# Optimization experiments

Measured on AMD Instinct MI355X. Metric: run time of the kernel, lower is better.

Reference implementation:

```python
import jax, jax.numpy as jnp
import numpy as np

B, T = 4, 2048
OBS, ST = 512, 512
H, E = 8, 64

def setup_inputs() -> dict:
    key = jax.random.key(0)
    k1, k2, k3, k4, k5 = jax.random.split(key, 5)
    observe = jax.random.normal(k1, (B, T, OBS), dtype=jnp.float32)
    state = jax.random.normal(k2, (B, T, ST), dtype=jnp.float32)
    # nn.Linear weights (out, in) applied as x @ W.T; store transposed for einsum
    Wq = jax.random.normal(k3, (OBS, H * E), dtype=jnp.float32) * (1.0 / np.sqrt(OBS))
    Wk = jax.random.normal(k4, (ST, H * E), dtype=jnp.float32) * (1.0 / np.sqrt(ST))
    Wv = jax.random.normal(k5, (ST, H * E), dtype=jnp.float32) * (1.0 / np.sqrt(ST))
    merge_w = jnp.ones((1, H, E), dtype=jnp.float32)  # Merger weight, init fill_(1.0)
    return {"observe": observe, "state": state, "Wq": Wq, "Wk": Wk, "Wv": Wv, "merge_w": merge_w}

def reference(observe, state, Wq, Wk, Wv, merge_w):
    b, t, _ = observe.shape
    h, e = H, E
    scale = e ** 0.25
    q = (observe @ Wq).reshape(b, t, h, e).transpose(0, 2, 1, 3) / scale  # [b,h,t,e]
    k = (state @ Wk).reshape(b, t, h, e).transpose(0, 2, 1, 3) / scale
    v = (state @ Wv).reshape(b, t, h, e).transpose(0, 2, 1, 3)
    dot = jnp.einsum('bhqe,bhke->bhqk', q, k)  # [b,h,t,t]
    attn = jax.nn.softmax(dot, axis=-1)
    out = jnp.einsum('bhqk,bhke->bhqe', attn, v)  # [b,h,t,e]
    out = out.transpose(0, 2, 1, 3).reshape(b * t, h, e)  # [b*t,h,e]
    # Merger: softmax over head dim of learned weight, weighted head sum
    w = jax.nn.softmax(merge_w, axis=1)  # [1,h,e]
    return jnp.sum(w * out, axis=1)  # [b*t,e]
```

## Files before the change

kernel.cpp:

```cpp
#include <hip/hip_runtime.h>

#define B_ 4
#define T_ 2048
#define H_ 8
#define E_ 64
#define KDIM 512

typedef unsigned short ushort_t;
typedef __attribute__((ext_vector_type(4))) float f32x4;
typedef __attribute__((ext_vector_type(4))) int i32x4;
typedef __attribute__((ext_vector_type(8))) short s16x8;

#define QK_SCALE 0.42466043f

__device__ __forceinline__ ushort_t f2bf(float f) {
  unsigned u = __builtin_bit_cast(unsigned, f);
  u += 0x7fffu + ((u >> 16) & 1u);
  return (ushort_t)(u >> 16);
}
__device__ __forceinline__ unsigned pk2(float a, float b) {
  return (unsigned)f2bf(a) | ((unsigned)f2bf(b) << 16);
}
__device__ __forceinline__ unsigned pk2t(float a, float b) {
  return __builtin_amdgcn_perm(__builtin_bit_cast(unsigned, b),
                               __builtin_bit_cast(unsigned, a), 0x07060302u);
}
__device__ __forceinline__ float e2(float x) { return __builtin_amdgcn_exp2f(x); }
__device__ __forceinline__ void gl2lds16(const void* g, void* l) {
  __builtin_amdgcn_global_load_lds((const __attribute__((address_space(1))) unsigned*)g,
                                   (__attribute__((address_space(3))) unsigned*)l, 16, 0, 0);
}

__global__ void k_prep(const float* __restrict__ Wq, const float* __restrict__ Wk,
                       const float* __restrict__ Wv, ushort_t* __restrict__ wt) {
  __shared__ ushort_t tile[64][66];
  int z = blockIdx.z;
  const float* W = (z == 0) ? Wq : (z == 1 ? Wk : Wv);
  float scale = (z < 2) ? QK_SCALE : 1.0f;
  int k0 = blockIdx.y << 6, n0 = blockIdx.x << 6;
  int rr = threadIdx.x >> 6, cc = threadIdx.x & 63;
  for (int p = 0; p < 16; p++) {
    int kl = p * 4 + rr;
    tile[cc][kl] = f2bf(W[(size_t)(k0 + kl) * 512 + n0 + cc] * scale);
  }
  __syncthreads();
  int kp2 = threadIdx.x & 31, nr = threadIdx.x >> 5;
  unsigned* wt32 = (unsigned*)(wt + (size_t)z * 262144);
  for (int p = 0; p < 8; p++) {
    int nl = p * 8 + nr;
    unsigned val = (unsigned)tile[nl][kp2 * 2] | ((unsigned)tile[nl][kp2 * 2 + 1] << 16);
    wt32[(size_t)(n0 + nl) * 256 + (k0 >> 1) + kp2] = val;
  }
}

__global__ void k_wgt(const float* __restrict__ mw, float* __restrict__ wgt) {
  int e = threadIdx.x;
  float w[8], wmax = -1e30f;
  for (int h = 0; h < 8; h++) { w[h] = mw[h * 64 + e]; wmax = fmaxf(wmax, w[h]); }
  float wsum = 0.f;
  for (int h = 0; h < 8; h++) { w[h] = __expf(w[h] - wmax); wsum += w[h]; }
  float inv = 1.f / wsum;
  for (int h = 0; h < 8; h++) wgt[h * 64 + e] = w[h] * inv;
}

__global__ void k_cvt(const float* __restrict__ obs, const float* __restrict__ st,
                      unsigned* __restrict__ xo, unsigned* __restrict__ xs) {
  int which = blockIdx.y;
  const float* src = which ? st : obs;
  unsigned* dst = which ? xs : xo;
  size_t idx = (size_t)blockIdx.x * 256 + threadIdx.x;
  size_t base = idx * 8;
  float4 x0 = *(const float4*)(src + base);
  float4 x1 = *(const float4*)(src + base + 4);
  uint4 d;
  d.x = pk2(x0.x, x0.y);
  d.y = pk2(x0.z, x0.w);
  d.z = pk2(x1.x, x1.y);
  d.w = pk2(x1.z, x1.w);
  *(uint4*)(dst + idx * 4) = d;
}

__global__ __launch_bounds__(256, 3) void k_proj2(
    const ushort_t* __restrict__ xo, const ushort_t* __restrict__ xs,
    const ushort_t* __restrict__ wt,
    ushort_t* __restrict__ qo, ushort_t* __restrict__ ko, ushort_t* __restrict__ vto) {
  __shared__ __align__(16) ushort_t As[2][128 * 64];

  int id = blockIdx.x;
  int xcd = id & 7, nt = (id >> 3) & 3, ghi = id >> 5;
  int g = ghi * 8 + xcd;
  int which = g >> 6, mb = g & 63;
  int m0 = mb << 7, n0 = nt << 7;
  const ushort_t* X = (which == 0) ? xo : xs;
  const ushort_t* W = wt + which * 262144;

  int tid = threadIdx.x, wave = tid >> 6, lane = tid & 63;
  int l15 = lane & 15, quad = lane >> 4;
  int wm = wave & 1, wn = wave >> 1;

  f32x4 acc[4][4];
  for (int i = 0; i < 4; i++)
    for (int j = 0; j < 4; j++) acc[i][j] = (f32x4){0.f, 0.f, 0.f, 0.f};

  int arl = lane >> 3, ap = lane & 7;

#define STAGEA(buf, k0)                                                            \
  do {                                                                             \
    for (int ii = 0; ii < 4; ii++) {                                               \
      int r = wave * 32 + ii * 8 + arl;                                            \
      gl2lds16(X + (size_t)(m0 + r) * KDIM + (k0) + ((ap ^ (r & 7)) << 3),         \
               &As[buf][(wave * 32 + ii * 8) * 64]);                               \
    }                                                                              \
  } while (0)

  const ushort_t* wb[4];
  for (int j = 0; j < 4; j++)
    wb[j] = W + (size_t)(n0 + wn * 64 + j * 16 + l15) * KDIM + quad * 8;

  STAGEA(0, 0);
  __builtin_amdgcn_s_waitcnt(0x0F70);
  __syncthreads();

  for (int kt = 0; kt < 8; kt++) {
    s16x8 b[2][4];
    for (int kc = 0; kc < 2; kc++)
      for (int j = 0; j < 4; j++) b[kc][j] = *(const s16x8*)(wb[j] + kc * 32);
    for (int j = 0; j < 4; j++) wb[j] += 64;
    if (kt < 7) STAGEA((kt + 1) & 1, kt * 64 + 64);
    const ushort_t* asb = As[kt & 1];
    for (int kc = 0; kc < 2; kc++) {
      s16x8 a[4];
      for (int i = 0; i < 4; i++) {
        int mr = wm * 64 + i * 16 + l15;
        int pc = (kc * 4 + quad) ^ (l15 & 7);
        a[i] = *(const s16x8*)&asb[mr * 64 + pc * 8];
      }
      if (which == 2) {
        for (int i = 0; i < 4; i++)
          for (int j = 0; j < 4; j++)
            acc[i][j] = __builtin_amdgcn_mfma_f32_16x16x32_bf16(b[kc][j], a[i], acc[i][j], 0, 0, 0);
      } else {
        for (int i = 0; i < 4; i++)
          for (int j = 0; j < 4; j++)
            acc[i][j] = __builtin_amdgcn_mfma_f32_16x16x32_bf16(a[i], b[kc][j], acc[i][j], 0, 0, 0);
      }
    }
    __builtin_amdgcn_s_waitcnt(0x0F70);
    __syncthreads();
  }
#undef STAGEA

  if (which != 2) {
    ushort_t* dst = (which == 0) ? qo : ko;
    for (int i = 0; i < 4; i++) {
      int grow = m0 + wm * 64 + i * 16 + quad * 4;
      for (int j = 0; j < 4; j++) {
        int gcol = n0 + wn * 64 + j * 16 + l15;
        int h = gcol >> 6, e = gcol & 63;
        for (int r = 0; r < 4; r++) {
          int row = grow + r;
          int bb = row >> 11, t = row & 2047;
          int bh = bb * H_ + h;
          dst[(((size_t)bh * T_ + t) << 6) + e] = f2bf(acc[i][j][r]);
        }
      }
    }
  } else {
    for (int i = 0; i < 4; i++) {
      int row = m0 + wm * 64 + i * 16 + l15;
      int bb = row >> 11, t = row & 2047;
      for (int j = 0; j < 4; j++) {
        for (int r = 0; r < 4; r++) {
          int gcol = n0 + wn * 64 + j * 16 + quad * 4 + r;
          int h = gcol >> 6, e = gcol & 63;
          int bh = bb * H_ + h;
          vto[((size_t)(bh << 6) + e) * T_ + t] = f2bf(acc[i][j][r]);
        }
      }
    }
  }
}

__global__ __launch_bounds__(256, 3) void k_proj(
    const float* __restrict__ obs, const float* __restrict__ st,
    const ushort_t* __restrict__ wt,
    ushort_t* __restrict__ qo, ushort_t* __restrict__ ko, ushort_t* __restrict__ vto) {
  __shared__ __align__(16) float As[2][128 * 32];

  int id = blockIdx.x;
  int xcd = id & 7, nt = (id >> 3) & 3, ghi = id >> 5;
  int g = ghi * 8 + xcd;
  int which = g >> 6, mb = g & 63;
  int m0 = mb << 7, n0 = nt << 7;
  const float* X = (which == 0) ? obs : st;
  const ushort_t* W = wt + which * 262144;

  int tid = threadIdx.x, wave = tid >> 6, lane = tid & 63;
  int l15 = lane & 15, quad = lane >> 4;
  int wm = wave & 1, wn = wave >> 1;

  f32x4 acc[4][4];
  for (int i = 0; i < 4; i++)
    for (int j = 0; j < 4; j++) acc[i][j] = (f32x4){0.f, 0.f, 0.f, 0.f};

  int arl = lane >> 3, ap = lane & 7;

#define STAGEA(buf, k0)                                                           \
  do {                                                                            \
    for (int ii = 0; ii < 4; ii++) {                                              \
      int r = wave * 32 + ii * 8 + arl;                                           \
      gl2lds16(X + (size_t)(m0 + r) * KDIM + (k0) + ((ap ^ (r & 7)) << 2),        \
               &As[buf][(wave * 32 + ii * 8) * 32]);                              \
    }                                                                             \
  } while (0)

  const ushort_t* wb[4];
  for (int j = 0; j < 4; j++)
    wb[j] = W + (size_t)(n0 + wn * 64 + j * 16 + l15) * KDIM + quad * 8;

  STAGEA(0, 0);
  __builtin_amdgcn_s_waitcnt(0x0F70);
  __syncthreads();

  for (int kt = 0; kt < 16; kt++) {
    s16x8 b[4];
    for (int j = 0; j < 4; j++) { b[j] = *(const s16x8*)wb[j]; wb[j] += 32; }
    if (kt < 15) STAGEA((kt + 1) & 1, kt * 32 + 32);
    const float* asb = As[kt & 1];
    s16x8 a[4];
    for (int i = 0; i < 4; i++) {
      int mr = wm * 64 + i * 16 + l15;
      int s = mr & 7;
      const float* rowp = &asb[mr * 32];
      float4 x0 = *(const float4*)&rowp[(((quad << 1)) ^ s) << 2];
      float4 x1 = *(const float4*)&rowp[(((quad << 1) | 1) ^ s) << 2];
      i32x4 d;
      d[0] = (int)pk2(x0.x, x0.y);
      d[1] = (int)pk2(x0.z, x0.w);
      d[2] = (int)pk2(x1.x, x1.y);
      d[3] = (int)pk2(x1.z, x1.w);
      a[i] = __builtin_bit_cast(s16x8, d);
    }
    if (which == 2) {
      for (int i = 0; i < 4; i++)
        for (int j = 0; j < 4; j++)
          acc[i][j] = __builtin_amdgcn_mfma_f32_16x16x32_bf16(b[j], a[i], acc[i][j], 0, 0, 0);
    } else {
      for (int i = 0; i < 4; i++)
        for (int j = 0; j < 4; j++)
          acc[i][j] = __builtin_amdgcn_mfma_f32_16x16x32_bf16(a[i], b[j], acc[i][j], 0, 0, 0);
    }
    __builtin_amdgcn_s_waitcnt(0x0F70);
    __syncthreads();
  }
#undef STAGEA

  if (which != 2) {
    ushort_t* dst = (which == 0) ? qo : ko;
    for (int i = 0; i < 4; i++) {
      int grow = m0 + wm * 64 + i * 16 + quad * 4;
      for (int j = 0; j < 4; j++) {
        int gcol = n0 + wn * 64 + j * 16 + l15;
        int h = gcol >> 6, e = gcol & 63;
        for (int r = 0; r < 4; r++) {
          int row = grow + r;
          int bb = row >> 11, t = row & 2047;
          int bh = bb * H_ + h;
          dst[(((size_t)bh * T_ + t) << 6) + e] = f2bf(acc[i][j][r]);
        }
      }
    }
  } else {
    for (int i = 0; i < 4; i++) {
      int row = m0 + wm * 64 + i * 16 + l15;
      int bb = row >> 11, t = row & 2047;
      for (int j = 0; j < 4; j++) {
        for (int r = 0; r < 4; r++) {
          int gcol = n0 + wn * 64 + j * 16 + quad * 4 + r;
          int h = gcol >> 6, e = gcol & 63;
          int bh = bb * H_ + h;
          vto[((size_t)(bh << 6) + e) * T_ + t] = f2bf(acc[i][j][r]);
        }
      }
    }
  }
}

union AttnSmem {
  struct { ushort_t ks[2][64 * 64]; ushort_t vs[2][64 * 64]; } st;
  struct { float ows[64 * 65]; float linv[64]; } ep;
};

__global__ __launch_bounds__(256, 4) void k_attn(
    const ushort_t* __restrict__ q, const ushort_t* __restrict__ k,
    const ushort_t* __restrict__ vt, const float* __restrict__ wgt,
    float* __restrict__ out) {
  __shared__ __align__(16) AttnSmem sm;

  int id = blockIdx.x;
  int bh = id & 31, qt = id >> 5;
  int tid = threadIdx.x, wave = tid >> 6, lane = tid & 63;
  int l15 = lane & 15, quad = lane >> 4;

  s16x8 qf[2][2];
  for (int qs = 0; qs < 2; qs++) {
    const ushort_t* qp =
        q + (((size_t)bh * T_ + qt * 128 + wave * 32 + qs * 16 + l15) << 6) + quad * 8;
    qf[qs][0] = *(const s16x8*)qp;
    qf[qs][1] = *(const s16x8*)(qp + 32);
  }
  int hh = bh & 7;
  float wgl = wgt[hh * 64 + lane];

  f32x4 o[2][4];
  for (int qs = 0; qs < 2; qs++)
    for (int j = 0; j < 4; j++) o[qs][j] = (f32x4){0.f, 0.f, 0.f, 0.f};
  f32x4 lacc[2] = {(f32x4){0.f, 0.f, 0.f, 0.f}, (f32x4){0.f, 0.f, 0.f, 0.f}};
  const s16x8 ones = {16256, 16256, 16256, 16256, 16256, 16256, 16256, 16256};

  int srl = lane >> 3, sp = lane & 7;
  const ushort_t* kbase = k + ((size_t)bh * T_ << 6);
  const ushort_t* vbase = vt + ((size_t)bh << 6) * T_;
  const ushort_t* kptr[2];
  const ushort_t* vptr[2];
  for (int ii = 0; ii < 2; ii++) {
    int r = wave * 16 + ii * 8 + srl;
    int gkey = (r & 32) + (((r >> 2) & 3) << 3) + (((r >> 4) & 1) << 2) + (r & 3);
    kptr[ii] = kbase + ((size_t)gkey << 6) + ((sp ^ (r & 7)) << 3);
    int e = r;
    vptr[ii] = vbase + (size_t)e * T_ + ((sp ^ (e & 7)) << 3);
  }

#define STAGE(buf)                                                         \
  do {                                                                     \
    for (int ii = 0; ii < 2; ii++) {                                       \
      gl2lds16(kptr[ii], &sm.st.ks[buf][(wave * 16 + ii * 8) * 64]);       \
      gl2lds16(vptr[ii], &sm.st.vs[buf][(wave * 16 + ii * 8) * 64]);       \
      kptr[ii] += 64 * 64;                                                 \
      vptr[ii] += 64;                                                      \
    }                                                                      \
  } while (0)

  STAGE(0);
  for (int kt = 0; kt < 32; kt++) {
    __builtin_amdgcn_s_waitcnt(0x0F70);
    __syncthreads();
    if (kt < 31) STAGE((kt + 1) & 1);
    const ushort_t* ksb = sm.st.ks[kt & 1];
    const ushort_t* vsb = sm.st.vs[kt & 1];

    s16x8 bfr[2][2];
    for (int c = 0; c < 2; c++) {
      f32x4 s0[2], s1[2];
      for (int qs = 0; qs < 2; qs++) {
        s0[qs] = (f32x4){0.f, 0.f, 0.f, 0.f};
        s1[qs] = (f32x4){0.f, 0.f, 0.f, 0.f};
      }
      for (int kc = 0; kc < 2; kc++) {
        int pc = (kc * 4 + quad) ^ (l15 & 7);
        s16x8 k0f = *(const s16x8*)&ksb[(c * 32 + l15) * 64 + pc * 8];
        s16x8 k1f = *(const s16x8*)&ksb[(c * 32 + 16 + l15) * 64 + pc * 8];
        for (int qs = 0; qs < 2; qs++) {
          s0[qs] = __builtin_amdgcn_mfma_f32_16x16x32_bf16(k0f, qf[qs][kc], s0[qs], 0, 0, 0);
          s1[qs] = __builtin_amdgcn_mfma_f32_16x16x32_bf16(k1f, qf[qs][kc], s1[qs], 0, 0, 0);
        }
      }
      for (int qs = 0; qs < 2; qs++) {
        i32x4 d;
        d[0] = (int)pk2t(e2(s0[qs][0]), e2(s0[qs][1]));
        d[1] = (int)pk2t(e2(s0[qs][2]), e2(s0[qs][3]));
        d[2] = (int)pk2t(e2(s1[qs][0]), e2(s1[qs][1]));
        d[3] = (int)pk2t(e2(s1[qs][2]), e2(s1[qs][3]));
        bfr[qs][c] = __builtin_bit_cast(s16x8, d);
      }
    }

    for (int c = 0; c < 2; c++) {
      lacc[0] = __builtin_amdgcn_mfma_f32_16x16x32_bf16(ones, bfr[0][c], lacc[0], 0, 0, 0);
      lacc[1] = __builtin_amdgcn_mfma_f32_16x16x32_bf16(ones, bfr[1][c], lacc[1], 0, 0, 0);
      for (int et = 0; et < 4; et++) {
        int pc = (c * 4 + quad) ^ (l15 & 7);
        s16x8 vf = *(const s16x8*)&vsb[(et * 16 + l15) * 64 + pc * 8];
        o[0][et] = __builtin_amdgcn_mfma_f32_16x16x32_bf16(vf, bfr[0][c], o[0][et], 0, 0, 0);
        o[1][et] = __builtin_amdgcn_mfma_f32_16x16x32_bf16(vf, bfr[1][c], o[1][et], 0, 0, 0);
      }
    }
  }
#undef STAGE

  int bb = bh >> 3;
  for (int half = 0; half < 2; half++) {
    __syncthreads();
    if ((wave >> 1) == half) {
      int tl = (wave & 1) * 32;
      for (int qs = 0; qs < 2; qs++) {
        int row = tl + qs * 16 + l15;
        if (quad == 0) sm.ep.linv[row] = 1.f / lacc[qs][0];
        for (int et = 0; et < 4; et++)
          for (int r = 0; r < 4; r++)
            sm.ep.ows[row * 65 + et * 16 + quad * 4 + r] = o[qs][et][r];
      }
    }
    __syncthreads();
    for (int i = 0; i < 16; i++) {
      int row = wave * 16 + i;
      int gt = qt * 128 + half * 64 + row;
      float val = sm.ep.ows[row * 65 + lane] * sm.ep.linv[row] * wgl;
      atomicAdd(&out[(((size_t)bb * T_ + gt) << 6) + lane], val);
    }
  }
}

extern "C" void kernel_launch(void* const* d_in, const int* in_sizes, int n_in,
                              void* d_out, int out_size, void* d_ws, size_t ws_size,
                              hipStream_t stream) {
  const float* obs = (const float*)d_in[0];
  const float* st  = (const float*)d_in[1];
  const float* Wq  = (const float*)d_in[2];
  const float* Wk  = (const float*)d_in[3];
  const float* Wv  = (const float*)d_in[4];
  const float* mw  = (const float*)d_in[5];

  const size_t WS_NEEDED = 27262976;
  const size_t WS_BIG    = 44040192;
  char* ws = (char*)d_ws;
  ushort_t* wt  = (ushort_t*)ws;
  float*    wgt = (float*)(ws + 1572864u);
  ushort_t* qo  = (ushort_t*)(ws + 2097152u);
  ushort_t* ko  = (ushort_t*)(ws + 10485760u);
  ushort_t* vto = (ushort_t*)(ws + 18874368u);
  ushort_t* xo  = (ushort_t*)(ws + 27262976u);
  ushort_t* xs  = (ushort_t*)(ws + 35651584u);
  float*    out = (float*)d_out;

  hipMemsetAsync(d_out, 0, (size_t)out_size * sizeof(float), stream);
  if (ws_size < WS_NEEDED) return;

  hipLaunchKernelGGL(k_prep, dim3(8, 8, 3), dim3(256), 0, stream, Wq, Wk, Wv, wt);
  hipLaunchKernelGGL(k_wgt,  dim3(1),       dim3(64),  0, stream, mw, wgt);
  if (ws_size >= WS_BIG) {
    hipLaunchKernelGGL(k_cvt,   dim3(2048, 2), dim3(256), 0, stream, obs, st,
                       (unsigned*)xo, (unsigned*)xs);
    hipLaunchKernelGGL(k_proj2, dim3(768),     dim3(256), 0, stream, xo, xs, wt, qo, ko, vto);
  } else {
    hipLaunchKernelGGL(k_proj,  dim3(768),     dim3(256), 0, stream, obs, st, wt, qo, ko, vto);
  }
  hipLaunchKernelGGL(k_attn, dim3(512), dim3(256), 0, stream, qo, ko, vto, wgt, out);
}
```

Before: 192.5 us.

## Triple-buffer LDS staging in projection and attention kernels with partial vmcnt waits

Both the projection GEMM and the attention kernel move from double to triple buffering of their LDS tiles, issuing loads two iterations ahead. They wait with a partial vmcnt so that only the oldest stage must land before the barrier, with raw s_barrier plus sched_barrier in place of __syncthreads. The goal is to hide more global-to-LDS latency behind MFMA work. In exchange LDS use grows, and the attention kernel's launch bounds drop from 4 to 2 blocks per CU, which may reduce occupancy.

```diff
diff --git a/kernel.cpp b/kernel.cpp
--- a/kernel.cpp
+++ b/kernel.cpp
@@ -84,7 +84,7 @@
     const ushort_t* __restrict__ xo, const ushort_t* __restrict__ xs,
     const ushort_t* __restrict__ wt,
     ushort_t* __restrict__ qo, ushort_t* __restrict__ ko, ushort_t* __restrict__ vto) {
-  __shared__ __align__(16) ushort_t As[2][128 * 64];
+  __shared__ __align__(16) ushort_t As[3][128 * 64];
 
   int id = blockIdx.x;
   int xcd = id & 7, nt = (id >> 3) & 3, ghi = id >> 5;
@@ -118,16 +118,22 @@
     wb[j] = W + (size_t)(n0 + wn * 64 + j * 16 + l15) * KDIM + quad * 8;
 
   STAGEA(0, 0);
-  __builtin_amdgcn_s_waitcnt(0x0F70);
-  __syncthreads();
-
+  STAGEA(1, 64);
+  __builtin_amdgcn_s_waitcnt(0x0F74);
+  __builtin_amdgcn_s_barrier();
+  __builtin_amdgcn_sched_barrier(0);
+
+#pragma unroll
   for (int kt = 0; kt < 8; kt++) {
     s16x8 b[2][4];
     for (int kc = 0; kc < 2; kc++)
       for (int j = 0; j < 4; j++) b[kc][j] = *(const s16x8*)(wb[j] + kc * 32);
     for (int j = 0; j < 4; j++) wb[j] += 64;
-    if (kt < 7) STAGEA((kt + 1) & 1, kt * 64 + 64);
-    const ushort_t* asb = As[kt & 1];
+    if (kt < 6) STAGEA((kt + 2) % 3, (kt + 2) * 64);
+    if (kt < 6) __builtin_amdgcn_s_waitcnt(0x0F74);
+    else        __builtin_amdgcn_s_waitcnt(0x0F70);
+    __builtin_amdgcn_sched_barrier(0);
+    const ushort_t* asb = As[kt % 3];
     for (int kc = 0; kc < 2; kc++) {
       s16x8 a[4];
       for (int i = 0; i < 4; i++) {
@@ -145,8 +151,10 @@
             acc[i][j] = __builtin_amdgcn_mfma_f32_16x16x32_bf16(a[i], b[kc][j], acc[i][j], 0, 0, 0);
       }
     }
-    __builtin_amdgcn_s_waitcnt(0x0F70);
-    __syncthreads();
+    if (kt < 7) {
+      __builtin_amdgcn_s_barrier();
+      __builtin_amdgcn_sched_barrier(0);
+    }
   }
 #undef STAGEA
 
@@ -287,11 +295,11 @@
 }
 
 union AttnSmem {
-  struct { ushort_t ks[2][64 * 64]; ushort_t vs[2][64 * 64]; } st;
+  struct { ushort_t ks[3][64 * 64]; ushort_t vs[3][64 * 64]; } st;
   struct { float ows[64 * 65]; float linv[64]; } ep;
 };
 
-__global__ __launch_bounds__(256, 4) void k_attn(
+__global__ __launch_bounds__(256, 2) void k_attn(
     const ushort_t* __restrict__ q, const ushort_t* __restrict__ k,
     const ushort_t* __restrict__ vt, const float* __restrict__ wgt,
     float* __restrict__ out) {
@@ -342,12 +350,16 @@
   } while (0)
 
   STAGE(0);
+  STAGE(1);
+  __builtin_amdgcn_s_waitcnt(0x0F74);
+  __builtin_amdgcn_s_barrier();
+  __builtin_amdgcn_sched_barrier(0);
+
+  int cur = 0, pre = 2;
   for (int kt = 0; kt < 32; kt++) {
-    __builtin_amdgcn_s_waitcnt(0x0F70);
-    __syncthreads();
-    if (kt < 31) STAGE((kt + 1) & 1);
-    const ushort_t* ksb = sm.st.ks[kt & 1];
-    const ushort_t* vsb = sm.st.vs[kt & 1];
+    if (kt < 30) STAGE(pre);
+    const ushort_t* ksb = &sm.st.ks[0][0] + cur * 4096;
+    const ushort_t* vsb = &sm.st.vs[0][0] + cur * 4096;
 
     s16x8 bfr[2][2];
     for (int c = 0; c < 2; c++) {
@@ -385,6 +397,15 @@
         o[1][et] = __builtin_amdgcn_mfma_f32_16x16x32_bf16(vf, bfr[1][c], o[1][et], 0, 0, 0);
       }
     }
+
+    if (kt < 30)       __builtin_amdgcn_s_waitcnt(0x0F74);
+    else if (kt == 30) __builtin_amdgcn_s_waitcnt(0x0F70);
+    if (kt < 31) {
+      __builtin_amdgcn_s_barrier();
+      __builtin_amdgcn_sched_barrier(0);
+    }
+    int nc = cur + 1; cur = (nc == 3) ? 0 : nc;
+    int np = pre + 1; pre = (np == 3) ? 0 : np;
   }
 #undef STAGE
 
```

Measured after the change: 186.3 us. 1.03x faster.
